# Kernel optimization log

Hardware: AMD Instinct MI355X
Metric: run time of the kernel (lower is better)

Reference implementation:

```python
import jax, jax.numpy as jnp
import numpy as np

N_NODES = 50000


def gcn_conv(x, src, dst, W, b):
    # PyG GCNConv: h = D^-1/2 (A+I) D^-1/2 (x W) + b, aggregation at dst.
    n = x.shape[0]
    deg = jax.ops.segment_sum(jnp.ones_like(dst, dtype=x.dtype), dst, num_segments=n)
    dinv = jnp.where(deg > 0, jax.lax.rsqrt(deg), 0.0)
    norm = dinv[src] * dinv[dst]                      # [E]
    h = x @ W                                         # [N, out]
    msg = h[src] * norm[:, None]                      # [E, out] gather
    out = jax.ops.segment_sum(msg, dst, num_segments=n)  # scatter-add
    return out + b


def setup_inputs() -> dict:
    key = jax.random.key(0)
    k1, k2, k3, k4 = jax.random.split(key, 4)
    in_dim, hid, out_dim = 128, 256, 128
    x = jax.random.normal(k1, (N_NODES, in_dim), dtype=jnp.float32)
    edge_index = jax.random.randint(k2, (2, 800000), 0, N_NODES, dtype=jnp.int64)
    s1 = 1.0 / np.sqrt(in_dim)
    s2 = 1.0 / np.sqrt(hid)
    W1 = jax.random.uniform(k3, (in_dim, hid), jnp.float32, -s1, s1)
    b1 = jnp.zeros((hid,), jnp.float32)
    W2 = jax.random.uniform(k4, (hid, out_dim), jnp.float32, -s2, s2)
    b2 = jnp.zeros((out_dim,), jnp.float32)
    return {"x": x, "edge_index": edge_index, "W1": W1, "b1": b1, "W2": W2, "b2": b2}


def reference(x, edge_index, W1, b1, W2, b2):
    n = x.shape[0]
    loops = jnp.arange(n, dtype=edge_index.dtype)
    src = jnp.concatenate([edge_index[0], loops])  # add self-loops
    dst = jnp.concatenate([edge_index[1], loops])
    h = jax.nn.relu(gcn_conv(x, src, dst, W1, b1))
    # dropout in eval mode -> identity
    return gcn_conv(h, src, dst, W2, b2)
```

## Files before the change

kernel.cpp:

```cpp
#include <hip/hip_runtime.h>
#include <hip/hip_bf16.h>


typedef __bf16 bf16x8v __attribute__((ext_vector_type(8)));
typedef short  s16x8   __attribute__((ext_vector_type(8)));
typedef float  f32x4   __attribute__((ext_vector_type(4)));

#define IN_DIM 128
#define HID    256
#define OUTD   128
#define BKT_SHIFT 7
#define BKT_NODES 128
#define MAXB 512
#define CAP  8192
#define EBLK 512

__device__ __forceinline__ float2 bf2f(__hip_bfloat162 v) {
    return make_float2(__bfloat162float(v.x), __bfloat162float(v.y));
}
__device__ __forceinline__ __hip_bfloat162 f2bf(float a, float b) {
    __hip_bfloat162 r; r.x = __float2bfloat16(a); r.y = __float2bfloat16(b); return r;
}
__device__ __forceinline__ void acc_row(float* acc, s16x8 r) {
    __hip_bfloat162* p = (__hip_bfloat162*)&r;
#pragma unroll
    for (int j = 0; j < 4; ++j) {
        float2 f = bf2f(p[j]);
        acc[2 * j]     += f.x;
        acc[2 * j + 1] += f.y;
    }
}

__global__ void k_detect(const void* W2raw, const void* eiraw, int* flags) {
    int lane = threadIdx.x;
    const unsigned short* u = (const unsigned short*)W2raw;
    unsigned e = (u[lane] >> 7) & 0xFF;
    unsigned long long m1 = __ballot(e >= 0x7F);
    const unsigned* ip = (const unsigned*)eiraw;
    unsigned long long m2 = __ballot(ip[2 * lane + 1] != 0);
    if (lane == 0) {
        flags[0] = (m1 != 0) ? 1 : 0;
        flags[1] = (m2 == 0) ? 1 : 0;
    }
}


__device__ __forceinline__ short ldw(const void* raw, int idx, int f32) {
    if (f32) {
        __hip_bfloat16 h = __float2bfloat16(((const float*)raw)[idx]);
        return *(short*)&h;
    }
    return ((const short*)raw)[idx];
}

template <int K, int NN>
__device__ __forceinline__ void swz_one(const void* Wraw, int f32,
                                        short* __restrict__ Bsw, int tid) {
    constexpr int KC = K / 32;
    constexpr int NT = NN / 16;
    if (tid >= NT * KC * 64) return;
    int lane = tid & 63;
    int kc   = (tid >> 6) % KC;
    int nt   = tid / (64 * KC);
    int n  = nt * 16 + (lane & 15);
    int kb = kc * 32 + (lane >> 4) * 8;
    s16x8 v;
#pragma unroll
    for (int j = 0; j < 8; ++j) v[j] = ldw(Wraw, (kb + j) * NN + n, f32);
    ((s16x8*)Bsw)[tid] = v;
}

__global__ __launch_bounds__(256) void k_prep_w(
        const void* W1raw, const void* b1raw, const void* W2raw, const void* b2raw,
        const int* __restrict__ flags, short* __restrict__ Bsw1, short* __restrict__ Bsw2,
        __hip_bfloat16* __restrict__ b1c, __hip_bfloat16* __restrict__ b2c) {
    int f32 = flags[0];
    int blk = blockIdx.x, t = threadIdx.x;
    if (blk < 16) {
        swz_one<IN_DIM, HID>(W1raw, f32, Bsw1, blk * 256 + t);
    } else if (blk < 32) {
        swz_one<HID, OUTD>(W2raw, f32, Bsw2, (blk - 16) * 256 + t);
    } else {
        short s1 = ldw(b1raw, t, f32);
        b1c[t] = *(__hip_bfloat16*)&s1;
        if (t < OUTD) {
            short s2 = ldw(b2raw, t, f32);
            b2c[t] = *(__hip_bfloat16*)&s2;
        }
    }
}


__global__ __launch_bounds__(256) void k_edges(
        const void* __restrict__ ei_, int E, int N, int NB,
        const int* __restrict__ flags, int* __restrict__ bcnt,
        unsigned* __restrict__ ppack) {
    __shared__ int lhist[4][MAXB];
    __shared__ int lbase[4][MAXB];
    int wv = threadIdx.x >> 6;
    int i64 = flags[1];
    const long long* p64 = (const long long*)ei_;
    const int*       p32 = (const int*)ei_;
    int per = (E + gridDim.x - 1) / gridDim.x;
    int e0 = blockIdx.x * per, e1 = min(e0 + per, E);
    for (int i = threadIdx.x; i < NB; i += 256) {
        lhist[0][i] = 0; lhist[1][i] = 0; lhist[2][i] = 0; lhist[3][i] = 0;
    }
    __syncthreads();
    for (int e = e0 + threadIdx.x; e < e1; e += 256) {
        int d = i64 ? (int)p64[E + e] : p32[E + e];
        if ((unsigned)d >= (unsigned)N) d = 0;
        atomicAdd(&lhist[wv][((unsigned)d) >> BKT_SHIFT], 1);
    }
    __syncthreads();
    for (int i = threadIdx.x; i < NB; i += 256) {
        int c0 = lhist[0][i], c1 = lhist[1][i], c2 = lhist[2][i], c3 = lhist[3][i];
        int tot = c0 + c1 + c2 + c3;
        int g = tot ? atomicAdd(&bcnt[i], tot) : 0;
        lbase[0][i] = g;
        lbase[1][i] = g + c0;
        lbase[2][i] = g + c0 + c1;
        lbase[3][i] = g + c0 + c1 + c2;
        lhist[0][i] = 0; lhist[1][i] = 0; lhist[2][i] = 0; lhist[3][i] = 0;
    }
    __syncthreads();
    for (int e = e0 + threadIdx.x; e < e1; e += 256) {
        int d = i64 ? (int)p64[E + e] : p32[E + e];
        int s = i64 ? (int)p64[e]     : p32[e];
        if ((unsigned)d >= (unsigned)N) d = 0;
        if ((unsigned)s >= (unsigned)N) s = 0;
        int b = ((unsigned)d) >> BKT_SHIFT;
        int pos = lbase[wv][b] + atomicAdd(&lhist[wv][b], 1);
        if (pos < CAP)
            ppack[(size_t)b * CAP + pos] = ((unsigned)(d & (BKT_NODES - 1)) << 25) | (unsigned)s;
    }
}

__global__ __launch_bounds__(512) void k_bscan(int* __restrict__ bcnt, int NB,
                                               int* __restrict__ boff,
                                               int* __restrict__ offsets, float* __restrict__ dinv,
                                               int N, int Npad) {
    __shared__ int s[MAXB];
    int t = threadIdx.x;
    int c = (t < NB) ? min(bcnt[t], CAP) : 0;
    if (t < NB) bcnt[t] = c;
    s[t] = c; __syncthreads();
    for (int off = 1; off < MAXB; off <<= 1) {
        int u = (t >= off) ? s[t - off] : 0;
        __syncthreads();
        s[t] += u;
        __syncthreads();
    }
    if (t < NB) boff[t] = s[t] - c;
    if (t == 0) { int tot = s[MAXB - 1]; boff[NB] = tot; offsets[N] = tot; }
    if (t < Npad - N) dinv[N + t] = 0.f;
}

__global__ __launch_bounds__(256) void k_bsort(const int* __restrict__ boff,
                                               const int* __restrict__ bcnt,
                                               const unsigned* __restrict__ ppack,
                                               int* __restrict__ csr, int* __restrict__ offsets,
                                               float* __restrict__ dinv, int N,
                                               const void* __restrict__ xraw,
                                               const int* __restrict__ flags,
                                               __hip_bfloat16* __restrict__ xs) {
    __shared__ int h[BKT_NODES], base[BKT_NODES], s[BKT_NODES];
    __shared__ float sdv[BKT_NODES];
    int b = blockIdx.x;
    int ebase = boff[b], cnt = bcnt[b];
    const unsigned* pp = ppack + (size_t)b * CAP;
    int t = threadIdx.x;
    if (t < BKT_NODES) h[t] = 0;
    __syncthreads();
    for (int e = t; e < cnt; e += 256) atomicAdd(&h[pp[e] >> 25], 1);
    __syncthreads();
    int v = (t < BKT_NODES) ? h[t] : 0;
    if (t < BKT_NODES) s[t] = v;
    __syncthreads();
    for (int off = 1; off < BKT_NODES; off <<= 1) {
        int u = (t < BKT_NODES && t >= off) ? s[t - off] : 0;
        __syncthreads();
        if (t < BKT_NODES) s[t] += u;
        __syncthreads();
    }
    if (t < BKT_NODES) {
        int excl = s[t] - v;
        base[t] = excl;
        int node = b * BKT_NODES + t;
        float dv = 0.f;
        if (node < N) {
            dv = rsqrtf((float)(v + 1));
            offsets[node] = ebase + excl;
            dinv[node] = dv;
        }
        sdv[t] = dv;
        h[t] = 0;
    }
    __syncthreads();
    for (int e = t; e < cnt; e += 256) {
        unsigned pk = pp[e];
        int ld = pk >> 25;
        int pos = ebase + base[ld] + atomicAdd(&h[ld], 1);
        csr[pos] = (int)(pk & 0x1FFFFFFu);
    }
    int f32 = flags[0];
    if (!f32) {
        const s16x8* xg = (const s16x8*)xraw;
        s16x8* xo = (s16x8*)xs;
        for (int u = t; u < BKT_NODES * 16; u += 256) {
            int row = u >> 4;
            int node = b * BKT_NODES + row;
            float dv = sdv[row];
            s16x8 val = {0, 0, 0, 0, 0, 0, 0, 0};
            if (node < N) {
                s16x8 xin = xg[(size_t)node * 16 + (u & 15)];
                __hip_bfloat162* xp = (__hip_bfloat162*)&xin;
                __hip_bfloat162* vp = (__hip_bfloat162*)&val;
#pragma unroll
                for (int j = 0; j < 4; ++j) {
                    float2 f = bf2f(xp[j]);
                    vp[j] = f2bf(dv * f.x, dv * f.y);
                }
            }
            xo[(size_t)node * 16 + (u & 15)] = val;
        }
    } else {
        const float4* xg = (const float4*)xraw;
        __hip_bfloat162* xo = (__hip_bfloat162*)xs;
        for (int u = t; u < BKT_NODES * 32; u += 256) {
            int row = u >> 5;
            int node = b * BKT_NODES + row;
            float dv = sdv[row];
            __hip_bfloat162 v0 = f2bf(0.f, 0.f), v1 = v0;
            if (node < N) {
                float4 xin = xg[(size_t)node * 32 + (u & 31)];
                v0 = f2bf(dv * xin.x, dv * xin.y);
                v1 = f2bf(dv * xin.z, dv * xin.w);
            }
            xo[(size_t)node * 64 + (u & 31) * 2]     = v0;
            xo[(size_t)node * 64 + (u & 31) * 2 + 1] = v1;
        }
    }
}


__global__ __launch_bounds__(256) void k_agg1(
        const s16x8* __restrict__ xs8, const int* __restrict__ offsets,
        const int* __restrict__ csr, const float* __restrict__ dinv,
        s16x8* __restrict__ a8, int N, int Npad, int nwaves) {
    int gw   = blockIdx.x * 4 + (threadIdx.x >> 6);
    int lane = threadIdx.x & 63;
    int g = lane >> 4, li = lane & 15;
    for (int v = gw; v < Npad; v += nwaves) {
        if (v >= N) {
            if (g == 0) { s16x8 z = {0,0,0,0,0,0,0,0}; a8[(size_t)v * 16 + li] = z; }
            continue;
        }
        float acc[8];
#pragma unroll
        for (int j = 0; j < 8; ++j) acc[j] = 0.f;
        int o0 = offsets[v], o1 = offsets[v + 1];
        if (g == 0) acc_row(acc, xs8[(size_t)v * 16 + li]);
        int e = o0 + g;
        for (; e + 4 < o1; e += 8) {
            int s0 = csr[e], s1 = csr[e + 4];
            s16x8 r0 = xs8[(size_t)s0 * 16 + li];
            s16x8 r1 = xs8[(size_t)s1 * 16 + li];
            acc_row(acc, r0);
            acc_row(acc, r1);
        }
        if (e < o1) acc_row(acc, xs8[(size_t)csr[e] * 16 + li]);
#pragma unroll
        for (int j = 0; j < 8; ++j) {
            acc[j] += __shfl_xor(acc[j], 16, 64);
            acc[j] += __shfl_xor(acc[j], 32, 64);
        }
        if (g == 0) {
            float dv = dinv[v];
            s16x8 outv;
            __hip_bfloat162* op = (__hip_bfloat162*)&outv;
#pragma unroll
            for (int j = 0; j < 4; ++j) op[j] = f2bf(dv * acc[2 * j], dv * acc[2 * j + 1]);
            a8[(size_t)v * 16 + li] = outv;
        }
    }
}


template <int K, int NN, bool RELU_BIAS>
__global__ __launch_bounds__(256) void k_gemm(
        const __hip_bfloat16* __restrict__ A, const __hip_bfloat16* __restrict__ Bsw,
        const __hip_bfloat16* __restrict__ bias, const float* __restrict__ dinv,
        __hip_bfloat16* __restrict__ C) {
    constexpr int KC = K / 32;
    constexpr int NT = NN / 16;
    int wave = threadIdx.x >> 6, lane = threadIdx.x & 63;
    int quad = lane >> 4, l16 = lane & 15;
    int m0 = blockIdx.x * 128 + wave * 32;

    bf16x8v a[2][KC];
#pragma unroll
    for (int st = 0; st < 2; ++st)
#pragma unroll
        for (int kc = 0; kc < KC; ++kc)
            a[st][kc] = *reinterpret_cast<const bf16x8v*>(
                A + (size_t)(m0 + st * 16 + l16) * K + kc * 32 + quad * 8);

    const bf16x8v* B8 = reinterpret_cast<const bf16x8v*>(Bsw);
    int rb0 = m0 + quad * 4, rb1 = m0 + 16 + quad * 4;
    float sc0[4], sc1[4];
    if (!RELU_BIAS) {
#pragma unroll
        for (int r = 0; r < 4; ++r) { sc0[r] = dinv[rb0 + r]; sc1[r] = dinv[rb1 + r]; }
    }

    for (int nt = 0; nt < NT; ++nt) {
        f32x4 acc0 = {0.f, 0.f, 0.f, 0.f}, acc1 = {0.f, 0.f, 0.f, 0.f};
#pragma unroll
        for (int kc = 0; kc < KC; ++kc) {
            bf16x8v bfrag = B8[(nt * KC + kc) * 64 + lane];
            acc0 = __builtin_amdgcn_mfma_f32_16x16x32_bf16(a[0][kc], bfrag, acc0, 0, 0, 0);
            acc1 = __builtin_amdgcn_mfma_f32_16x16x32_bf16(a[1][kc], bfrag, acc1, 0, 0, 0);
        }
        int col = nt * 16 + l16;
        if (RELU_BIAS) {
            float bv = __bfloat162float(bias[col]);
#pragma unroll
            for (int r = 0; r < 4; ++r) {
                float v0 = acc0[r] + bv; v0 = v0 > 0.f ? v0 : 0.f;
                float v1 = acc1[r] + bv; v1 = v1 > 0.f ? v1 : 0.f;
                C[(size_t)(rb0 + r) * NN + col] = __float2bfloat16(v0);
                C[(size_t)(rb1 + r) * NN + col] = __float2bfloat16(v1);
            }
        } else {
#pragma unroll
            for (int r = 0; r < 4; ++r) {
                C[(size_t)(rb0 + r) * NN + col] = __float2bfloat16(acc0[r] * sc0[r]);
                C[(size_t)(rb1 + r) * NN + col] = __float2bfloat16(acc1[r] * sc1[r]);
            }
        }
    }
}


__global__ __launch_bounds__(256) void k_agg2(
        const s16x8* __restrict__ h8, const int* __restrict__ offsets,
        const int* __restrict__ csr, const float* __restrict__ dinv,
        const __hip_bfloat16* __restrict__ b2c, const int* __restrict__ flags,
        void* __restrict__ outraw, int N, int nwaves) {
    int gw   = blockIdx.x * 4 + (threadIdx.x >> 6);
    int lane = threadIdx.x & 63;
    int g = lane >> 4, li = lane & 15;
    int f32 = flags[0];
    float bb[8];
    {
        s16x8 bv = ((const s16x8*)b2c)[li];
        __hip_bfloat162* bp = (__hip_bfloat162*)&bv;
#pragma unroll
        for (int j = 0; j < 4; ++j) {
            float2 f = bf2f(bp[j]);
            bb[2 * j] = f.x; bb[2 * j + 1] = f.y;
        }
    }
    for (int v = gw; v < N; v += nwaves) {
        float acc[8];
#pragma unroll
        for (int j = 0; j < 8; ++j) acc[j] = 0.f;
        int o0 = offsets[v], o1 = offsets[v + 1];
        if (g == 0) acc_row(acc, h8[(size_t)v * 16 + li]);
        int e = o0 + g;
        for (; e + 4 < o1; e += 8) {
            int s0 = csr[e], s1 = csr[e + 4];
            s16x8 r0 = h8[(size_t)s0 * 16 + li];
            s16x8 r1 = h8[(size_t)s1 * 16 + li];
            acc_row(acc, r0);
            acc_row(acc, r1);
        }
        if (e < o1) acc_row(acc, h8[(size_t)csr[e] * 16 + li]);
#pragma unroll
        for (int j = 0; j < 8; ++j) {
            acc[j] += __shfl_xor(acc[j], 16, 64);
            acc[j] += __shfl_xor(acc[j], 32, 64);
        }
        if (g == 0) {
            float dv = dinv[v];
            if (f32) {
                float4* of = (float4*)outraw;
                float4 o0v = {dv * acc[0] + bb[0], dv * acc[1] + bb[1],
                              dv * acc[2] + bb[2], dv * acc[3] + bb[3]};
                float4 o1v = {dv * acc[4] + bb[4], dv * acc[5] + bb[5],
                              dv * acc[6] + bb[6], dv * acc[7] + bb[7]};
                of[(size_t)v * 32 + li * 2]     = o0v;
                of[(size_t)v * 32 + li * 2 + 1] = o1v;
            } else {
                s16x8 outv;
                __hip_bfloat162* op = (__hip_bfloat162*)&outv;
#pragma unroll
                for (int j = 0; j < 4; ++j)
                    op[j] = f2bf(dv * acc[2 * j] + bb[2 * j], dv * acc[2 * j + 1] + bb[2 * j + 1]);
                ((s16x8*)outraw)[(size_t)v * 16 + li] = outv;
            }
        }
    }
}


extern "C" void kernel_launch(void* const* d_in, const int* in_sizes, int n_in,
                              void* d_out, int out_size, void* d_ws, size_t ws_size,
                              hipStream_t stream) {
    const void* x  = d_in[0];
    const void* ei = d_in[1];
    const void* W1 = d_in[2];
    const void* b1 = d_in[3];
    const void* W2 = d_in[4];
    const void* b2 = d_in[5];

    const int N = in_sizes[0] / IN_DIM;
    const int E = in_sizes[1] / 2;
    const int Npad = ((N + 127) / 128) * 128;
    const int NB = (N + BKT_NODES - 1) / BKT_NODES;

    char* w = (char*)d_ws;
    auto alloc = [&](size_t bytes) -> void* {
        void* p = (void*)w;
        w += (bytes + 255) / 256 * 256;
        return p;
    };
    int*   flags   = (int*)alloc(256);
    int*   bcnt    = (int*)alloc((size_t)MAXB * 4);
    int*   boff    = (int*)alloc((size_t)(MAXB + 1) * 4);
    int*   offsets = (int*)alloc((size_t)(N + 1) * 4);
    float* dinv    = (float*)alloc((size_t)Npad * 4);
    unsigned* ppack = (unsigned*)alloc((size_t)NB * CAP * 4);
    int*   csr     = (int*)alloc((size_t)E * 4);
    short* Bsw1 = (short*)alloc((size_t)IN_DIM * HID * 2);
    short* Bsw2 = (short*)alloc((size_t)HID * OUTD * 2);
    __hip_bfloat16* b1c = (__hip_bfloat16*)alloc((size_t)HID * 2);
    __hip_bfloat16* b2c = (__hip_bfloat16*)alloc((size_t)OUTD * 2);
    __hip_bfloat16* xs  = (__hip_bfloat16*)alloc((size_t)Npad * IN_DIM * 2);
    __hip_bfloat16* a1  = (__hip_bfloat16*)alloc((size_t)Npad * IN_DIM * 2);
    __hip_bfloat16* h1  = (__hip_bfloat16*)alloc((size_t)Npad * HID * 2);
    __hip_bfloat16* h2s = xs;

    k_detect<<<1, 64, 0, stream>>>(W2, ei, flags);
    hipMemsetAsync(bcnt, 0, (size_t)MAXB * 4, stream);

    k_prep_w<<<33, 256, 0, stream>>>(W1, b1, W2, b2, flags, Bsw1, Bsw2, b1c, b2c);

    k_edges<<<EBLK, 256, 0, stream>>>(ei, E, N, NB, flags, bcnt, ppack);
    k_bscan<<<1, MAXB, 0, stream>>>(bcnt, NB, boff, offsets, dinv, N, Npad);
    k_bsort<<<NB, 256, 0, stream>>>(boff, bcnt, ppack, csr, offsets, dinv, N,
                                    x, flags, xs);

    const int aggBlocks = 2048, nwaves = aggBlocks * 4;
    k_agg1<<<aggBlocks, 256, 0, stream>>>((const s16x8*)xs, offsets, csr, dinv,
                                          (s16x8*)a1, N, Npad, nwaves);

    k_gemm<IN_DIM, HID, true><<<Npad / 128, 256, 0, stream>>>(
        a1, (const __hip_bfloat16*)Bsw1, b1c, nullptr, h1);
    k_gemm<HID, OUTD, false><<<Npad / 128, 256, 0, stream>>>(
        h1, (const __hip_bfloat16*)Bsw2, nullptr, dinv, h2s);

    k_agg2<<<aggBlocks, 256, 0, stream>>>((const s16x8*)h2s, offsets, csr, dinv,
                                          b2c, flags, d_out, N, nwaves);
}
```

Baseline: 224.2 us.

## Fuse the two GEMMs through LDS, merge small setup kernels, unroll aggregation

The layer-1 and layer-2 GEMMs become one kernel that keeps the 128x256 ReLU hidden tile in swizzled LDS instead of writing h1 to global memory and reading it back. The bucket prefix scan is folded into k_bsort, each block re-scanning the bucket counts, and format detection is folded into k_prep_w, which removes two tiny launches. k_bsort now runs with 512 threads. The aggregation loops are unrolled to four gathers in flight. The fused GEMM uses 64 KB of LDS per block, which limits occupancy, and the redundant per-block scan adds some work.

Measured after the change: 220.1 us. Within noise of the previous version (-1.8%).

```diff
diff --git a/kernel.cpp b/kernel.cpp
--- a/kernel.cpp
+++ b/kernel.cpp
@@ -31,17 +31,15 @@
     }
 }
 
-__global__ void k_detect(const void* W2raw, const void* eiraw, int* flags) {
-    int lane = threadIdx.x;
+__device__ __forceinline__ int detect_f32(const void* W2raw) {
     const unsigned short* u = (const unsigned short*)W2raw;
-    unsigned e = (u[lane] >> 7) & 0xFF;
-    unsigned long long m1 = __ballot(e >= 0x7F);
-    const unsigned* ip = (const unsigned*)eiraw;
-    unsigned long long m2 = __ballot(ip[2 * lane + 1] != 0);
-    if (lane == 0) {
-        flags[0] = (m1 != 0) ? 1 : 0;
-        flags[1] = (m2 == 0) ? 1 : 0;
-    }
+    int f32 = 0;
+#pragma unroll
+    for (int i = 0; i < 64; ++i) {
+        unsigned e = (u[i] >> 7) & 0xFF;
+        if (e >= 0x7F) f32 = 1;
+    }
+    return f32;
 }
 
 
@@ -72,9 +70,10 @@
 
 __global__ __launch_bounds__(256) void k_prep_w(
         const void* W1raw, const void* b1raw, const void* W2raw, const void* b2raw,
-        const int* __restrict__ flags, short* __restrict__ Bsw1, short* __restrict__ Bsw2,
-        __hip_bfloat16* __restrict__ b1c, __hip_bfloat16* __restrict__ b2c) {
-    int f32 = flags[0];
+        const void* eiraw, short* __restrict__ Bsw1, short* __restrict__ Bsw2,
+        __hip_bfloat16* __restrict__ b1c, __hip_bfloat16* __restrict__ b2c,
+        int* __restrict__ flags) {
+    int f32 = detect_f32(W2raw);
     int blk = blockIdx.x, t = threadIdx.x;
     if (blk < 16) {
         swz_one<IN_DIM, HID>(W1raw, f32, Bsw1, blk * 256 + t);
@@ -86,6 +85,14 @@
         if (t < OUTD) {
             short s2 = ldw(b2raw, t, f32);
             b2c[t] = *(__hip_bfloat16*)&s2;
+        }
+        if (t == 0) {
+            const unsigned* ip = (const unsigned*)eiraw;
+            unsigned orodd = 0;
+#pragma unroll
+            for (int i = 0; i < 64; ++i) orodd |= ip[2 * i + 1];
+            flags[0] = f32;
+            flags[1] = (orodd == 0) ? 1 : 0;
         }
     }
 }
@@ -136,43 +143,36 @@
     }
 }
 
-__global__ __launch_bounds__(512) void k_bscan(int* __restrict__ bcnt, int NB,
-                                               int* __restrict__ boff,
-                                               int* __restrict__ offsets, float* __restrict__ dinv,
-                                               int N, int Npad) {
-    __shared__ int s[MAXB];
-    int t = threadIdx.x;
-    int c = (t < NB) ? min(bcnt[t], CAP) : 0;
-    if (t < NB) bcnt[t] = c;
-    s[t] = c; __syncthreads();
-    for (int off = 1; off < MAXB; off <<= 1) {
-        int u = (t >= off) ? s[t - off] : 0;
-        __syncthreads();
-        s[t] += u;
-        __syncthreads();
-    }
-    if (t < NB) boff[t] = s[t] - c;
-    if (t == 0) { int tot = s[MAXB - 1]; boff[NB] = tot; offsets[N] = tot; }
-    if (t < Npad - N) dinv[N + t] = 0.f;
-}
-
-__global__ __launch_bounds__(256) void k_bsort(const int* __restrict__ boff,
-                                               const int* __restrict__ bcnt,
+
+__global__ __launch_bounds__(512) void k_bsort(const int* __restrict__ bcnt,
                                                const unsigned* __restrict__ ppack,
+                                               int NB,
                                                int* __restrict__ csr, int* __restrict__ offsets,
                                                float* __restrict__ dinv, int N,
                                                const void* __restrict__ xraw,
                                                const int* __restrict__ flags,
                                                __hip_bfloat16* __restrict__ xs) {
+    __shared__ int sb[MAXB];
     __shared__ int h[BKT_NODES], base[BKT_NODES], s[BKT_NODES];
     __shared__ float sdv[BKT_NODES];
     int b = blockIdx.x;
-    int ebase = boff[b], cnt = bcnt[b];
+    int t = threadIdx.x;
+    int c = (t < NB) ? min(bcnt[t], CAP) : 0;
+    sb[t] = c;
+    __syncthreads();
+    for (int off = 1; off < MAXB; off <<= 1) {
+        int u = (t >= off) ? sb[t - off] : 0;
+        __syncthreads();
+        sb[t] += u;
+        __syncthreads();
+    }
+    int cnt   = min(bcnt[b], CAP);
+    int ebase = sb[b] - cnt;
+    if (b == NB - 1 && t == 0) offsets[N] = sb[b];
     const unsigned* pp = ppack + (size_t)b * CAP;
-    int t = threadIdx.x;
     if (t < BKT_NODES) h[t] = 0;
     __syncthreads();
-    for (int e = t; e < cnt; e += 256) atomicAdd(&h[pp[e] >> 25], 1);
+    for (int e = t; e < cnt; e += 512) atomicAdd(&h[pp[e] >> 25], 1);
     __syncthreads();
     int v = (t < BKT_NODES) ? h[t] : 0;
     if (t < BKT_NODES) s[t] = v;
@@ -192,12 +192,14 @@
             dv = rsqrtf((float)(v + 1));
             offsets[node] = ebase + excl;
             dinv[node] = dv;
+        } else {
+            dinv[node] = 0.f;
         }
         sdv[t] = dv;
         h[t] = 0;
     }
     __syncthreads();
-    for (int e = t; e < cnt; e += 256) {
+    for (int e = t; e < cnt; e += 512) {
         unsigned pk = pp[e];
         int ld = pk >> 25;
         int pos = ebase + base[ld] + atomicAdd(&h[ld], 1);
@@ -207,7 +209,7 @@
     if (!f32) {
         const s16x8* xg = (const s16x8*)xraw;
         s16x8* xo = (s16x8*)xs;
-        for (int u = t; u < BKT_NODES * 16; u += 256) {
+        for (int u = t; u < BKT_NODES * 16; u += 512) {
             int row = u >> 4;
             int node = b * BKT_NODES + row;
             float dv = sdv[row];
@@ -227,7 +229,7 @@
     } else {
         const float4* xg = (const float4*)xraw;
         __hip_bfloat162* xo = (__hip_bfloat162*)xs;
-        for (int u = t; u < BKT_NODES * 32; u += 256) {
+        for (int u = t; u < BKT_NODES * 32; u += 512) {
             int row = u >> 5;
             int node = b * BKT_NODES + row;
             float dv = sdv[row];
@@ -262,14 +264,15 @@
         int o0 = offsets[v], o1 = offsets[v + 1];
         if (g == 0) acc_row(acc, xs8[(size_t)v * 16 + li]);
         int e = o0 + g;
-        for (; e + 4 < o1; e += 8) {
-            int s0 = csr[e], s1 = csr[e + 4];
+        for (; e + 12 < o1; e += 16) {
+            int s0 = csr[e], s1 = csr[e + 4], s2 = csr[e + 8], s3 = csr[e + 12];
             s16x8 r0 = xs8[(size_t)s0 * 16 + li];
             s16x8 r1 = xs8[(size_t)s1 * 16 + li];
-            acc_row(acc, r0);
-            acc_row(acc, r1);
-        }
-        if (e < o1) acc_row(acc, xs8[(size_t)csr[e] * 16 + li]);
+            s16x8 r2 = xs8[(size_t)s2 * 16 + li];
+            s16x8 r3 = xs8[(size_t)s3 * 16 + li];
+            acc_row(acc, r0); acc_row(acc, r1); acc_row(acc, r2); acc_row(acc, r3);
+        }
+        for (; e < o1; e += 4) acc_row(acc, xs8[(size_t)csr[e] * 16 + li]);
 #pragma unroll
         for (int j = 0; j < 8; ++j) {
             acc[j] += __shfl_xor(acc[j], 16, 64);
@@ -287,57 +290,75 @@
 }
 
 
-template <int K, int NN, bool RELU_BIAS>
-__global__ __launch_bounds__(256) void k_gemm(
-        const __hip_bfloat16* __restrict__ A, const __hip_bfloat16* __restrict__ Bsw,
-        const __hip_bfloat16* __restrict__ bias, const float* __restrict__ dinv,
-        __hip_bfloat16* __restrict__ C) {
-    constexpr int KC = K / 32;
-    constexpr int NT = NN / 16;
+__global__ __launch_bounds__(256) void k_gemm12(
+        const __hip_bfloat16* __restrict__ A, const __hip_bfloat16* __restrict__ Bsw1,
+        const __hip_bfloat16* __restrict__ b1c, const __hip_bfloat16* __restrict__ Bsw2,
+        const float* __restrict__ dinv, __hip_bfloat16* __restrict__ h2s) {
+    __shared__ __align__(16) __hip_bfloat16 hl[128 * HID];
     int wave = threadIdx.x >> 6, lane = threadIdx.x & 63;
     int quad = lane >> 4, l16 = lane & 15;
-    int m0 = blockIdx.x * 128 + wave * 32;
-
-    bf16x8v a[2][KC];
+    int mw = wave * 32;
+    int gm = blockIdx.x * 128 + mw;
+
+    bf16x8v a1f[2][4];
 #pragma unroll
     for (int st = 0; st < 2; ++st)
 #pragma unroll
-        for (int kc = 0; kc < KC; ++kc)
-            a[st][kc] = *reinterpret_cast<const bf16x8v*>(
-                A + (size_t)(m0 + st * 16 + l16) * K + kc * 32 + quad * 8);
-
-    const bf16x8v* B8 = reinterpret_cast<const bf16x8v*>(Bsw);
-    int rb0 = m0 + quad * 4, rb1 = m0 + 16 + quad * 4;
+        for (int kc = 0; kc < 4; ++kc)
+            a1f[st][kc] = *reinterpret_cast<const bf16x8v*>(
+                A + (size_t)(gm + st * 16 + l16) * IN_DIM + kc * 32 + quad * 8);
+
+    const bf16x8v* B1 = reinterpret_cast<const bf16x8v*>(Bsw1);
+    for (int nt = 0; nt < HID / 16; ++nt) {
+        f32x4 acc0 = {0.f, 0.f, 0.f, 0.f}, acc1 = {0.f, 0.f, 0.f, 0.f};
+#pragma unroll
+        for (int kc = 0; kc < 4; ++kc) {
+            bf16x8v bfrag = B1[(nt * 4 + kc) * 64 + lane];
+            acc0 = __builtin_amdgcn_mfma_f32_16x16x32_bf16(a1f[0][kc], bfrag, acc0, 0, 0, 0);
+            acc1 = __builtin_amdgcn_mfma_f32_16x16x32_bf16(a1f[1][kc], bfrag, acc1, 0, 0, 0);
+        }
+        int col = nt * 16 + l16;
+        int gcol = col >> 3, csub = col & 7;
+        float bv = __bfloat162float(b1c[col]);
+#pragma unroll
+        for (int r = 0; r < 4; ++r) {
+            float v0 = acc0[r] + bv; v0 = v0 > 0.f ? v0 : 0.f;
+            float v1 = acc1[r] + bv; v1 = v1 > 0.f ? v1 : 0.f;
+            int r0 = mw + quad * 4 + r;
+            int r1 = mw + 16 + quad * 4 + r;
+            ((__hip_bfloat16*)((char*)hl + (size_t)r0 * (HID * 2) + ((gcol ^ (r0 & 31)) << 4)))[csub] = __float2bfloat16(v0);
+            ((__hip_bfloat16*)((char*)hl + (size_t)r1 * (HID * 2) + ((gcol ^ (r1 & 31)) << 4)))[csub] = __float2bfloat16(v1);
+        }
+    }
+
+    bf16x8v a2f[2][8];
+#pragma unroll
+    for (int st = 0; st < 2; ++st)
+#pragma unroll
+        for (int kc = 0; kc < 8; ++kc) {
+            int row = mw + st * 16 + l16;
+            int g = (kc * 4 + quad) ^ (row & 31);
+            a2f[st][kc] = *reinterpret_cast<const bf16x8v*>(
+                (char*)hl + (size_t)row * (HID * 2) + ((size_t)g << 4));
+        }
+    const bf16x8v* B2 = reinterpret_cast<const bf16x8v*>(Bsw2);
+    int rb0 = gm + quad * 4, rb1 = gm + 16 + quad * 4;
     float sc0[4], sc1[4];
-    if (!RELU_BIAS) {
-#pragma unroll
-        for (int r = 0; r < 4; ++r) { sc0[r] = dinv[rb0 + r]; sc1[r] = dinv[rb1 + r]; }
-    }
-
-    for (int nt = 0; nt < NT; ++nt) {
+#pragma unroll
+    for (int r = 0; r < 4; ++r) { sc0[r] = dinv[rb0 + r]; sc1[r] = dinv[rb1 + r]; }
+    for (int nt = 0; nt < OUTD / 16; ++nt) {
         f32x4 acc0 = {0.f, 0.f, 0.f, 0.f}, acc1 = {0.f, 0.f, 0.f, 0.f};
 #pragma unroll
-        for (int kc = 0; kc < KC; ++kc) {
-            bf16x8v bfrag = B8[(nt * KC + kc) * 64 + lane];
-            acc0 = __builtin_amdgcn_mfma_f32_16x16x32_bf16(a[0][kc], bfrag, acc0, 0, 0, 0);
-            acc1 = __builtin_amdgcn_mfma_f32_16x16x32_bf16(a[1][kc], bfrag, acc1, 0, 0, 0);
+        for (int kc = 0; kc < 8; ++kc) {
+            bf16x8v bfrag = B2[(nt * 8 + kc) * 64 + lane];
+            acc0 = __builtin_amdgcn_mfma_f32_16x16x32_bf16(a2f[0][kc], bfrag, acc0, 0, 0, 0);
+            acc1 = __builtin_amdgcn_mfma_f32_16x16x32_bf16(a2f[1][kc], bfrag, acc1, 0, 0, 0);
         }
         int col = nt * 16 + l16;
-        if (RELU_BIAS) {
-            float bv = __bfloat162float(bias[col]);
-#pragma unroll
-            for (int r = 0; r < 4; ++r) {
-                float v0 = acc0[r] + bv; v0 = v0 > 0.f ? v0 : 0.f;
-                float v1 = acc1[r] + bv; v1 = v1 > 0.f ? v1 : 0.f;
-                C[(size_t)(rb0 + r) * NN + col] = __float2bfloat16(v0);
-                C[(size_t)(rb1 + r) * NN + col] = __float2bfloat16(v1);
-            }
-        } else {
-#pragma unroll
-            for (int r = 0; r < 4; ++r) {
-                C[(size_t)(rb0 + r) * NN + col] = __float2bfloat16(acc0[r] * sc0[r]);
-                C[(size_t)(rb1 + r) * NN + col] = __float2bfloat16(acc1[r] * sc1[r]);
-            }
+#pragma unroll
+        for (int r = 0; r < 4; ++r) {
+            h2s[(size_t)(rb0 + r) * OUTD + col] = __float2bfloat16(acc0[r] * sc0[r]);
+            h2s[(size_t)(rb1 + r) * OUTD + col] = __float2bfloat16(acc1[r] * sc1[r]);
         }
     }
 }
@@ -369,14 +390,15 @@
         int o0 = offsets[v], o1 = offsets[v + 1];
         if (g == 0) acc_row(acc, h8[(size_t)v * 16 + li]);
         int e = o0 + g;
-        for (; e + 4 < o1; e += 8) {
-            int s0 = csr[e], s1 = csr[e + 4];
+        for (; e + 12 < o1; e += 16) {
+            int s0 = csr[e], s1 = csr[e + 4], s2 = csr[e + 8], s3 = csr[e + 12];
             s16x8 r0 = h8[(size_t)s0 * 16 + li];
             s16x8 r1 = h8[(size_t)s1 * 16 + li];
-            acc_row(acc, r0);
-            acc_row(acc, r1);
-        }
-        if (e < o1) acc_row(acc, h8[(size_t)csr[e] * 16 + li]);
+            s16x8 r2 = h8[(size_t)s2 * 16 + li];
+            s16x8 r3 = h8[(size_t)s3 * 16 + li];
+            acc_row(acc, r0); acc_row(acc, r1); acc_row(acc, r2); acc_row(acc, r3);
+        }
+        for (; e < o1; e += 4) acc_row(acc, h8[(size_t)csr[e] * 16 + li]);
 #pragma unroll
         for (int j = 0; j < 8; ++j) {
             acc[j] += __shfl_xor(acc[j], 16, 64);
@@ -418,7 +440,7 @@
     const int N = in_sizes[0] / IN_DIM;
     const int E = in_sizes[1] / 2;
     const int Npad = ((N + 127) / 128) * 128;
-    const int NB = (N + BKT_NODES - 1) / BKT_NODES;
+    const int NB = Npad / BKT_NODES;
 
     char* w = (char*)d_ws;
     auto alloc = [&](size_t bytes) -> void* {
@@ -428,7 +450,6 @@
     };
     int*   flags   = (int*)alloc(256);
     int*   bcnt    = (int*)alloc((size_t)MAXB * 4);
-    int*   boff    = (int*)alloc((size_t)(MAXB + 1) * 4);
     int*   offsets = (int*)alloc((size_t)(N + 1) * 4);
     float* dinv    = (float*)alloc((size_t)Npad * 4);
     unsigned* ppack = (unsigned*)alloc((size_t)NB * CAP * 4);
@@ -439,27 +460,21 @@
     __hip_bfloat16* b2c = (__hip_bfloat16*)alloc((size_t)OUTD * 2);
     __hip_bfloat16* xs  = (__hip_bfloat16*)alloc((size_t)Npad * IN_DIM * 2);
     __hip_bfloat16* a1  = (__hip_bfloat16*)alloc((size_t)Npad * IN_DIM * 2);
-    __hip_bfloat16* h1  = (__hip_bfloat16*)alloc((size_t)Npad * HID * 2);
     __hip_bfloat16* h2s = xs;
 
-    k_detect<<<1, 64, 0, stream>>>(W2, ei, flags);
+    k_prep_w<<<33, 256, 0, stream>>>(W1, b1, W2, b2, ei, Bsw1, Bsw2, b1c, b2c, flags);
     hipMemsetAsync(bcnt, 0, (size_t)MAXB * 4, stream);
 
-    k_prep_w<<<33, 256, 0, stream>>>(W1, b1, W2, b2, flags, Bsw1, Bsw2, b1c, b2c);
-
     k_edges<<<EBLK, 256, 0, stream>>>(ei, E, N, NB, flags, bcnt, ppack);
-    k_bscan<<<1, MAXB, 0, stream>>>(bcnt, NB, boff, offsets, dinv, N, Npad);
-    k_bsort<<<NB, 256, 0, stream>>>(boff, bcnt, ppack, csr, offsets, dinv, N,
+    k_bsort<<<NB, 512, 0, stream>>>(bcnt, ppack, NB, csr, offsets, dinv, N,
                                     x, flags, xs);
 
     const int aggBlocks = 2048, nwaves = aggBlocks * 4;
     k_agg1<<<aggBlocks, 256, 0, stream>>>((const s16x8*)xs, offsets, csr, dinv,
                                           (s16x8*)a1, N, Npad, nwaves);
 
-    k_gemm<IN_DIM, HID, true><<<Npad / 128, 256, 0, stream>>>(
-        a1, (const __hip_bfloat16*)Bsw1, b1c, nullptr, h1);
-    k_gemm<HID, OUTD, false><<<Npad / 128, 256, 0, stream>>>(
-        h1, (const __hip_bfloat16*)Bsw2, nullptr, dinv, h2s);
+    k_gemm12<<<NB, 256, 0, stream>>>(a1, (const __hip_bfloat16*)Bsw1, b1c,
+                                     (const __hip_bfloat16*)Bsw2, dinv, h2s);
 
     k_agg2<<<aggBlocks, 256, 0, stream>>>((const s16x8*)h2s, offsets, csr, dinv,
                                           b2c, flags, d_out, N, nwaves);
```
